# Optimization experiments

Hardware: AMD Instinct MI355X
Metric: run time of the kernel (lower is better)

## Reference

```python
import jax, jax.numpy as jnp
import numpy as np

NV, NF, DIM = 6144, 12288, 256


def _linear(x, W, b):
    # torch nn.Linear: x @ W.T + b, W has shape (out, in)
    return x @ W.T + b


def _agg(X, A, Wf, bf, Wg, bg):
    # AGG: out_fc = Linear(A @ X); out_gagg = Linear(A @ out_fc)  (eval mode: dropout is identity)
    out_fc = _linear(A @ X, Wf, bf)
    out_g = _linear(A @ out_fc, Wg, bg)
    return jax.nn.relu(out_fc + out_g)


def setup_inputs() -> dict:
    key = jax.random.key(0)
    ks = jax.random.split(key, 18)
    primal = jax.random.normal(ks[0], (NV, DIM), jnp.float32)
    # degree-normalized adjacency (docstring): scale uniform entries by 1/N for stable row sums
    A_primal = jax.random.uniform(ks[1], (NV, NV), jnp.float32) * (1.0 / NV)
    A_dual = jax.random.uniform(ks[2], (NF, NF), jnp.float32) * (1.0 / NF)
    A = jax.random.uniform(ks[3], (NV, NF), jnp.float32) * (1.0 / NF)
    faces = jax.random.randint(ks[4], (NF, 3), 0, NV)

    w = lambda k, shp: jax.random.normal(k, shp, jnp.float32) * 0.05
    return {
        "primal": primal, "A_primal": A_primal, "A_dual": A_dual, "A": A, "faces": faces,
        # 3 primal AGG layers (fc + gagg), stacked on leading axis
        "pW": w(ks[5], (3, DIM, DIM)), "pb": w(ks[6], (3, DIM)),
        "pgW": w(ks[7], (3, DIM, DIM)), "pgb": w(ks[8], (3, DIM)),
        # 3 dual AGG layers
        "dW": w(ks[9], (3, DIM, DIM)), "db": w(ks[10], (3, DIM)),
        "dgW": w(ks[11], (3, DIM, DIM)), "dgb": w(ks[12], (3, DIM)),
        # PDF linears: (dim, 2*dim)
        "Wp": w(ks[13], (DIM, 2 * DIM)), "bp": w(ks[14], (DIM,)),
        "Wd": w(ks[15], (DIM, 2 * DIM)), "bd": w(ks[16], (DIM,)),
    }


def reference(primal, A_primal, A_dual, A, faces, pW, pb, pgW, pgb, dW, db, dgW, dgb, Wp, bp, Wd, bd):
    x_p = primal
    x_d = (1.0 / 3.0) * (A.T @ primal)  # primal_dual
    primal_outs, dual_outs = [], []
    for i in range(3):
        primal_outs.append(x_p)
        x_p = _agg(x_p, A_primal, pW[i], pb[i], pgW[i], pgb[i]) + x_p
    for i in range(3):
        dual_outs.append(x_d)
        x_d = _agg(x_d, A_dual, dW[i], db[i], dgW[i], dgb[i]) + x_d
    # PDF: DAP gather-reduce  (N_f, 3, dim) -> (N_f, dim)
    f = jnp.mean(jnp.abs(x_p[faces] - x_d[:, None, :]), axis=1)
    out_dual = jax.nn.relu(_linear(jnp.concatenate([x_d, f], axis=1), Wd, bd))
    mapped = A @ f  # dual_primal
    out_primal = jax.nn.relu(_linear(jnp.concatenate([x_p, mapped], axis=1), Wp, bp))
    return (out_primal + x_p, out_dual + x_d, *primal_outs, *dual_outs)
```

## Files before the change

### kernel.cpp

```cpp
#include <hip/hip_runtime.h>


typedef short short8 __attribute__((ext_vector_type(8)));
typedef float floatx4 __attribute__((ext_vector_type(4)));
typedef unsigned short ushort4v __attribute__((ext_vector_type(4)));
typedef unsigned short u16;

#define DIMN 256
#define GBK 64

static const int kNV = 6144;
static const int kNF = 12288;
static const int SLAB = 768;

#define RW_PW    0
#define RW_PGW   1572864
#define RW_DW    3145728
#define RW_DGW   3932160
#define RW_WCOMB 4718592
#define RW_TOT   5308416

__device__ __forceinline__ float bf2f(u16 u) {
  union { unsigned int i; float f; } x; x.i = ((unsigned int)u) << 16; return x.f;
}
__device__ __forceinline__ u16 f2bf(float f) {
  union { float f; unsigned int i; } x; x.f = f;
  unsigned int r = x.i + 0x7fffu + ((x.i >> 16) & 1u);
  return (u16)(r >> 16);
}
__device__ __forceinline__ void gld_lds16(const void* g, void* l) {
  __builtin_amdgcn_global_load_lds((__attribute__((address_space(1))) void*)(g),
                                   (__attribute__((address_space(3))) void*)(l),
                                   16, 0, 0);
}

__global__ __launch_bounds__(256, 2)
void gemm_bf16_k(const void* __restrict__ A0, int A0is32, size_t aslab0,
                 const void* __restrict__ A1, int A1is32, size_t aslab1, int K1,
                 int lda0, int lda1,
                 const void* __restrict__ Bt, int Btis32, int ldb,
                 void* __restrict__ P, int M, int nx, int kchunk,
                 int fused, const float* __restrict__ bias,
                 const u16* __restrict__ addmat, int do_relu,
                 const float* __restrict__ resid,
                 float* __restrict__ outf, u16* __restrict__ out16)
{
  __shared__ __align__(16) u16 As[2][128 * GBK];
  __shared__ __align__(16) u16 Bs[2][128 * GBK];

  const int nwg = gridDim.x;
  const int d = ((blockIdx.x & 7) * (nwg >> 3)) + (blockIdx.x >> 3);
  const int y = d & 1;
  const int bx = (d >> 1) % nx;
  const int bz = (d >> 1) / nx;
  const int m0 = bx << 7;
  const int n0 = y << 7;
  const int kb = bz * kchunk;
  const int nkt = kchunk / GBK;

  const int tid = threadIdx.x;
  const int wid = tid >> 6;
  const int lane = tid & 63;
  const int wr = wid >> 1, wc = wid & 1;
  const int srow = lane >> 3;
  const int skk = (lane & 7) << 3;

  floatx4 acc[4][4];
  floatx4 zz = {0.f, 0.f, 0.f, 0.f};
#pragma unroll
  for (int i = 0; i < 4; ++i)
#pragma unroll
    for (int j = 0; j < 4; ++j) acc[i][j] = zz;

  auto stage = [&](int buf, int k0) {
    const void* base; int lda, is32, kl; size_t aslab;
    if (k0 < K1) { base = A0; lda = lda0; is32 = A0is32; kl = k0; aslab = aslab0; }
    else { base = A1; lda = lda1; is32 = A1is32; kl = k0 - K1; aslab = aslab1; }
    const size_t koff = aslab ? ((size_t)(kl >> 8) * aslab + (kl & 255)) : (size_t)kl;
    if (is32) {
      const float* F = (const float*)base;
#pragma unroll
      for (int j = 0; j < 4; ++j) {
        int c = (wid << 2) + j;
        const size_t gi = (size_t)(m0 + (c << 3) + srow) * lda + koff + skk;
        floatx4 f0 = *(const floatx4*)(F + gi);
        floatx4 f1 = *(const floatx4*)(F + gi + 4);
        short8 v;
#pragma unroll
        for (int e = 0; e < 4; ++e) { v[e] = (short)f2bf(f0[e]); v[4 + e] = (short)f2bf(f1[e]); }
        *(short8*)&As[buf][(c << 9) + (lane << 3)] = v;
      }
    } else {
      const u16* U = (const u16*)base;
#pragma unroll
      for (int j = 0; j < 4; ++j) {
        int c = (wid << 2) + j;
        gld_lds16(U + (size_t)(m0 + (c << 3) + srow) * lda + koff + skk,
                  (void*)&As[buf][c << 9]);
      }
    }
    if (Btis32) {
      const float* F = (const float*)Bt;
#pragma unroll
      for (int j = 0; j < 4; ++j) {
        int c = (wid << 2) + j;
        const size_t gi = (size_t)(n0 + (c << 3) + srow) * ldb + k0 + skk;
        floatx4 f0 = *(const floatx4*)(F + gi);
        floatx4 f1 = *(const floatx4*)(F + gi + 4);
        short8 v;
#pragma unroll
        for (int e = 0; e < 4; ++e) { v[e] = (short)f2bf(f0[e]); v[4 + e] = (short)f2bf(f1[e]); }
        *(short8*)&Bs[buf][(c << 9) + (lane << 3)] = v;
      }
    } else {
      const u16* U = (const u16*)Bt;
#pragma unroll
      for (int j = 0; j < 4; ++j) {
        int c = (wid << 2) + j;
        gld_lds16(U + (size_t)(n0 + (c << 3) + srow) * ldb + k0 + skk,
                  (void*)&Bs[buf][c << 9]);
      }
    }
  };

  int cur = 0;
  stage(0, kb);
  for (int kt = 0; kt < nkt; ++kt) {
    __syncthreads();
    if (kt + 1 < nkt) stage(cur ^ 1, kb + (kt + 1) * GBK);
#pragma unroll
    for (int ks = 0; ks < 2; ++ks) {
      short8 a[4], b[4];
      const int ko = (ks << 5) + ((lane >> 4) << 3);
#pragma unroll
      for (int mi = 0; mi < 4; ++mi)
        a[mi] = *(const short8*)&As[cur][((wr << 6) + (mi << 4) + (lane & 15)) * GBK + ko];
#pragma unroll
      for (int ni = 0; ni < 4; ++ni)
        b[ni] = *(const short8*)&Bs[cur][((wc << 6) + (ni << 4) + (lane & 15)) * GBK + ko];
#pragma unroll
      for (int mi = 0; mi < 4; ++mi)
#pragma unroll
        for (int ni = 0; ni < 4; ++ni)
          acc[mi][ni] = __builtin_amdgcn_mfma_f32_16x16x32_bf16(a[mi], b[ni], acc[mi][ni], 0, 0, 0);
    }
    cur ^= 1;
  }

  if (fused) {
#pragma unroll
    for (int mi = 0; mi < 4; ++mi) {
#pragma unroll
      for (int ni = 0; ni < 4; ++ni) {
        const int mb = m0 + (wr << 6) + (mi << 4) + ((lane >> 4) << 2);
        const int n = n0 + (wc << 6) + (ni << 4) + (lane & 15);
        const float bv = bias ? bias[n] : 0.f;
#pragma unroll
        for (int r = 0; r < 4; ++r) {
          const size_t idx = (size_t)(mb + r) * DIMN + n;
          float t = acc[mi][ni][r] + bv;
          if (addmat) t += bf2f(addmat[idx]);
          if (do_relu) t = fmaxf(t, 0.f);
          if (resid) t += resid[idx];
          if (outf) outf[idx] = t;
          if (out16) out16[idx] = f2bf(t);
        }
      }
    }
  } else {
    u16* Pz = (u16*)P + (size_t)bz * (size_t)M * DIMN;
#pragma unroll
    for (int mi = 0; mi < 4; ++mi) {
#pragma unroll
      for (int ni = 0; ni < 4; ++ni) {
        const int mb = m0 + (wr << 6) + (mi << 4) + ((lane >> 4) << 2);
        const int n = n0 + (wc << 6) + (ni << 4) + (lane & 15);
#pragma unroll
        for (int r = 0; r < 4; ++r)
          Pz[(size_t)(mb + r) * DIMN + n] = f2bf(acc[mi][ni][r]);
      }
    }
  }
}

__global__ __launch_bounds__(256)
void finalize_k(const u16* __restrict__ P, int S, int Mrows, float scale,
                float* __restrict__ out, u16* __restrict__ out16)
{
  const size_t MN = (size_t)Mrows * DIMN;
  const size_t i4 = (((size_t)blockIdx.x * blockDim.x) + threadIdx.x) * 4;
  if (i4 >= MN) return;
  floatx4 v = {0.f, 0.f, 0.f, 0.f};
  for (int s = 0; s < S; ++s) {
    ushort4v p4 = *(const ushort4v*)(P + (size_t)s * MN + i4);
#pragma unroll
    for (int j = 0; j < 4; ++j) v[j] += bf2f(p4[j]);
  }
  floatx4 o;
#pragma unroll
  for (int j = 0; j < 4; ++j) o[j] = v[j] * scale;
  if (out) *(floatx4*)(out + i4) = o;
  if (out16) {
    unsigned long long q = 0;
#pragma unroll
    for (int j = 0; j < 4; ++j) q |= ((unsigned long long)f2bf(o[j])) << (16 * j);
    *(unsigned long long*)(out16 + i4) = q;
  }
}

__global__ __launch_bounds__(256)
void finalize_tr_k(const u16* __restrict__ P, int S, int Mrows, float scale,
                   float* __restrict__ outf, u16* __restrict__ outT, int ldT)
{
  __shared__ __align__(16) u16 t[64][64];
  const size_t MN = (size_t)Mrows * DIMN;
  const int r0 = blockIdx.x << 6;
  const int c0 = blockIdx.y << 6;
  const int tid = threadIdx.x;
  const int lr = tid >> 3;
  const int lc = (tid & 7) << 3;
#pragma unroll
  for (int h = 0; h < 2; ++h) {
    const int r = lr + (h << 5);
    const size_t gi = (size_t)(r0 + r) * DIMN + (c0 + lc);
    float a[8];
#pragma unroll
    for (int e = 0; e < 8; ++e) a[e] = 0.f;
    for (int s = 0; s < S; ++s) {
      short8 p = *(const short8*)(P + (size_t)s * MN + gi);
#pragma unroll
      for (int e = 0; e < 8; ++e) a[e] += bf2f((u16)p[e]);
    }
    short8 v;
    floatx4 o0, o1;
#pragma unroll
    for (int e = 0; e < 4; ++e) {
      o0[e] = a[e] * scale; o1[e] = a[4 + e] * scale;
      v[e] = (short)f2bf(o0[e]); v[4 + e] = (short)f2bf(o1[e]);
    }
    *(floatx4*)(outf + gi) = o0;
    *(floatx4*)(outf + gi + 4) = o1;
    *(short8*)&t[r][lc ^ ((r >> 3) << 3)] = v;
  }
  __syncthreads();
#pragma unroll
  for (int h = 0; h < 2; ++h) {
    const int oc = lr + (h << 5);
    short8 v;
#pragma unroll
    for (int e = 0; e < 8; ++e)
      v[e] = (short)t[lc + e][oc ^ ((lc >> 3) << 3)];
    *(short8*)&outT[(size_t)(c0 + oc) * ldT + (r0 + lc)] = v;
  }
}

__global__ __launch_bounds__(256)
void transpose_k(const void* __restrict__ in, int is32, int ldin,
                 u16* __restrict__ out, int ldout, u16* __restrict__ copy16)
{
  __shared__ __align__(16) u16 t[64][64];
  const int c0 = blockIdx.x << 6;
  const int r0 = blockIdx.y << 6;
  const int tid = threadIdx.x;
  const int lr = tid >> 3;
  const int lc = (tid & 7) << 3;
#pragma unroll
  for (int h = 0; h < 2; ++h) {
    const int r = lr + (h << 5);
    short8 v;
    if (is32) {
      const float* F = (const float*)in;
      const size_t gi = (size_t)(r0 + r) * ldin + (c0 + lc);
      floatx4 f0 = *(const floatx4*)(F + gi);
      floatx4 f1 = *(const floatx4*)(F + gi + 4);
#pragma unroll
      for (int e = 0; e < 4; ++e) { v[e] = (short)f2bf(f0[e]); v[4 + e] = (short)f2bf(f1[e]); }
      if (copy16) *(short8*)(copy16 + gi) = v;
    } else {
      v = *(const short8*)((const u16*)in + (size_t)(r0 + r) * ldin + (c0 + lc));
    }
    *(short8*)&t[r][lc ^ ((r >> 3) << 3)] = v;
  }
  __syncthreads();
#pragma unroll
  for (int h = 0; h < 2; ++h) {
    const int oc = lr + (h << 5);
    short8 v;
#pragma unroll
    for (int e = 0; e < 8; ++e)
      v[e] = (short)t[lc + e][oc ^ ((lc >> 3) << 3)];
    *(short8*)&out[(size_t)(c0 + oc) * ldout + (r0 + lc)] = v;
  }
}

__global__ __launch_bounds__(256)
void cvt8_k(const float* __restrict__ in, u16* __restrict__ out, size_t n)
{
  const size_t stride = (size_t)gridDim.x * 2048;
  for (size_t i = (((size_t)blockIdx.x << 8) + threadIdx.x) << 3; i < n; i += stride) {
    floatx4 f0 = *(const floatx4*)(in + i);
    floatx4 f1 = *(const floatx4*)(in + i + 4);
    short8 v;
#pragma unroll
    for (int e = 0; e < 4; ++e) { v[e] = (short)f2bf(f0[e]); v[4 + e] = (short)f2bf(f1[e]); }
    *(short8*)(out + i) = v;
  }
}

__global__ __launch_bounds__(256)
void repw_k(const float* __restrict__ pW, const float* __restrict__ pgW,
            const float* __restrict__ dW, const float* __restrict__ dgW,
            const float* __restrict__ Wp, u16* __restrict__ arena)
{
  const size_t o = (((size_t)blockIdx.x << 8) + threadIdx.x) << 3;
  if (o >= RW_TOT) return;
  const float* src;
  size_t so;
  if (o < RW_PGW) {
    size_t r = o - RW_PW; int i = (int)(r >> 19); int rr = (int)(r & 524287);
    so = (size_t)i * 65536 + (rr >> 11) * 256 + (rr & 255); src = pW;
  } else if (o < RW_DW) {
    size_t r = o - RW_PGW; int i = (int)(r >> 19); int rr = (int)(r & 524287);
    so = (size_t)i * 65536 + (rr >> 11) * 256 + (rr & 255); src = pgW;
  } else if (o < RW_DGW) {
    size_t r = o - RW_DW; int i = (int)(r >> 18); int rr = (int)(r & 262143);
    so = (size_t)i * 65536 + (rr >> 10) * 256 + (rr & 255); src = dW;
  } else if (o < RW_WCOMB) {
    size_t r = o - RW_DGW; int i = (int)(r >> 18); int rr = (int)(r & 262143);
    so = (size_t)i * 65536 + (rr >> 10) * 256 + (rr & 255); src = dgW;
  } else {
    size_t r = o - RW_WCOMB; int n = (int)(r / 2304); int k2 = (int)(r % 2304);
    so = (size_t)n * 512 + ((k2 < 256) ? k2 : (256 + ((k2 - 256) & 255))); src = Wp;
  }
  short8 v;
#pragma unroll
  for (int e = 0; e < 8; ++e) v[e] = (short)f2bf(src[so + e]);
  *(short8*)(arena + o) = v;
}

__global__ __launch_bounds__(256)
void face_gather_k(const float* __restrict__ xp, const float* __restrict__ xd,
                   const int* __restrict__ faces, u16* __restrict__ f)
{
  const int fi = blockIdx.x;
  const int j = threadIdx.x;
  const int a = faces[fi * 3 + 0];
  const int b = faces[fi * 3 + 1];
  const int c = faces[fi * 3 + 2];
  const float xv = xd[(size_t)fi * DIMN + j];
  const float s = fabsf(xp[(size_t)a * DIMN + j] - xv)
                + fabsf(xp[(size_t)b * DIMN + j] - xv)
                + fabsf(xp[(size_t)c * DIMN + j] - xv);
  f[(size_t)fi * DIMN + j] = f2bf(s * (1.0f / 3.0f));
}

extern "C" void kernel_launch(void* const* d_in, const int* in_sizes, int n_in,
                              void* d_out, int out_size, void* d_ws, size_t ws_size,
                              hipStream_t stream)
{
  (void)in_sizes; (void)n_in; (void)out_size;
  const float* primal   = (const float*)d_in[0];
  const float* A_primal = (const float*)d_in[1];
  const float* A_dual   = (const float*)d_in[2];
  const float* A        = (const float*)d_in[3];
  const int* faces      = (const int*)d_in[4];
  const float* pW  = (const float*)d_in[5];
  const float* pb  = (const float*)d_in[6];
  const float* pgW = (const float*)d_in[7];
  const float* pgb = (const float*)d_in[8];
  const float* dW  = (const float*)d_in[9];
  const float* db  = (const float*)d_in[10];
  const float* dgW = (const float*)d_in[11];
  const float* dgb = (const float*)d_in[12];
  const float* Wp  = (const float*)d_in[13];
  const float* bp  = (const float*)d_in[14];
  const float* Wd  = (const float*)d_in[15];
  const float* bd  = (const float*)d_in[16];

  char* wsp = (char*)d_ws;
  auto alloc = [&](size_t bytes) -> void* {
    void* p = (void*)wsp;
    wsp += (bytes + 255) & ~(size_t)255;
    return p;
  };
  const size_t NVD = (size_t)kNV * DIMN, NFD = (size_t)kNF * DIMN;
  u16* XT    = (u16*)alloc(NFD * 2);
  u16* TB    = (u16*)alloc((size_t)SLAB * kNV * 2);
  u16* t1    = (u16*)alloc(NFD * 2);
  u16* fc    = (u16*)alloc(NFD * 2);
  u16* P     = (u16*)alloc((size_t)8 * NFD * 2);
  u16* Wrep  = (u16*)alloc((size_t)RW_TOT * 2);
  const size_t bigElems = (size_t)kNF * kNF + 2 * (size_t)kNF * kNV + (size_t)kNV * kNV;
  const size_t need = (size_t)(wsp - (char*)d_ws) + bigElems * 2 + 4096;
  const bool big = ws_size >= need;
  u16 *Ad16 = nullptr, *At16 = nullptr, *A16 = nullptr, *Ap16 = nullptr;
  if (big) {
    Ad16 = (u16*)alloc((size_t)kNF * kNF * 2);
    At16 = (u16*)alloc((size_t)kNF * kNV * 2);
    A16  = (u16*)alloc((size_t)kNV * kNF * 2);
    Ap16 = (u16*)alloc((size_t)kNV * kNV * 2);
  }

  float* out0  = (float*)d_out;
  float* out1  = out0 + NVD;
  float* pouts = out1 + NFD;
  float* douts = pouts + 3 * NVD;

  auto gemmP = [&](const void* A0p, int a0is32, int lda0,
                   const void* Btp, int ldb, int M, int K, int S) {
    const int nx = M / 128;
    gemm_bf16_k<<<dim3(nx * 2 * S), dim3(256), 0, stream>>>(
        A0p, a0is32, 0, nullptr, 0, 0, K, lda0, 0, Btp, 0, ldb,
        P, M, nx, K / S, 0, nullptr, nullptr, 0, nullptr, nullptr, nullptr);
  };
  auto gemmF = [&](const void* A0p, int a0is32, size_t as0, int lda0,
                   const void* A1p, int a1is32, size_t as1, int lda1, int K1,
                   const void* Btp, int btis32, int ldb, int M, int K,
                   const float* bias, const u16* add, int relu,
                   const float* resid, float* outf, u16* out16) {
    const int nx = M / 128;
    gemm_bf16_k<<<dim3(nx * 2), dim3(256), 0, stream>>>(
        A0p, a0is32, as0, A1p, a1is32, as1, K1, lda0, lda1, Btp, btis32, ldb,
        P, M, nx, K, 1, bias, add, relu, resid, outf, out16);
  };
  auto tranp = [&](const void* in, int is32, int ldin, u16* out, int ldout,
                   int R, int C, u16* copy16) {
    transpose_k<<<dim3(C / 64, R / 64), dim3(256), 0, stream>>>(
        in, is32, ldin, out, ldout, copy16);
  };
  auto cvt = [&](const float* in, u16* out, size_t n) {
    cvt8_k<<<dim3(2048), dim3(256), 0, stream>>>(in, out, n);
  };

  repw_k<<<dim3(RW_TOT / 2048), dim3(256), 0, stream>>>(pW, pgW, dW, dgW, Wp, Wrep);
  if (big) {
    cvt(A_dual, Ad16, (size_t)kNF * kNF);
    cvt(A_primal, Ap16, (size_t)kNV * kNV);
    tranp(A, 1, kNF, At16, kNV, kNV, kNF, A16);
  }
  tranp(primal, 1, DIMN, XT, kNV, kNV, DIMN, nullptr);
  hipMemcpyAsync(pouts, primal, NVD * 4, hipMemcpyDeviceToDevice, stream);

  const void* ApP = big ? (const void*)Ap16 : (const void*)A_primal;
  const int apf = big ? 0 : 1;
  const void* AdP = big ? (const void*)Ad16 : (const void*)A_dual;
  const int adf = big ? 0 : 1;

  const float* xpc = primal;
  for (int i = 0; i < 3; ++i) {
    gemmP(ApP, apf, kNV, XT, kNV, kNV, kNV, 8);
    gemmF(P, 0, NVD, 256, nullptr, 0, 0, 0, 2048,
          Wrep + RW_PW + (size_t)i * 524288, 0, 2048, kNV, 2048,
          pb + i * 256, nullptr, 0, nullptr, nullptr, fc);
    tranp(fc, 0, DIMN, TB, kNV, kNV, DIMN, nullptr);
    gemmP(ApP, apf, kNV, TB, kNV, kNV, kNV, 8);
    float* nxt = (i < 2) ? (pouts + (size_t)(i + 1) * NVD) : out0;
    gemmF(P, 0, NVD, 256, nullptr, 0, 0, 0, 2048,
          Wrep + RW_PGW + (size_t)i * 524288, 0, 2048, kNV, 2048,
          pgb + i * 256, fc, 1, xpc, nxt, nullptr);
    xpc = nxt;
    if (i < 2) tranp(xpc, 1, DIMN, XT, kNV, kNV, DIMN, nullptr);
  }

  if (big) {
    tranp(primal, 1, DIMN, XT, kNV, kNV, DIMN, nullptr);
    gemmP(At16, 0, kNV, XT, kNV, kNF, kNV, 4);
    finalize_tr_k<<<dim3(kNF / 64, 4), dim3(256), 0, stream>>>(
        P, 4, kNF, 1.0f / 3.0f, douts, XT, kNF);
  } else {
    tranp(primal, 1, DIMN, XT, kNV, kNV, DIMN, nullptr);
    for (int s = 0; s < kNF / SLAB; ++s) {
      const int m0 = s * SLAB;
      tranp(A + m0, 1, kNF, TB, kNV, kNV, SLAB, nullptr);
      gemmP(TB, 0, kNV, XT, kNV, SLAB, kNV, 16);
      finalize_k<<<dim3((unsigned)((size_t)SLAB * DIMN / 1024)), dim3(256), 0, stream>>>(
          P, 16, SLAB, 1.0f / 3.0f, douts + (size_t)m0 * DIMN, nullptr);
    }
    tranp(douts, 1, DIMN, XT, kNF, kNF, DIMN, nullptr);
  }

  const float* xdc = douts;
  for (int i = 0; i < 3; ++i) {
    gemmP(AdP, adf, kNF, XT, kNF, kNF, kNF, 4);
    gemmF(P, 0, NFD, 256, nullptr, 0, 0, 0, 1024,
          Wrep + RW_DW + (size_t)i * 262144, 0, 1024, kNF, 1024,
          db + i * 256, nullptr, 0, nullptr, nullptr, fc);
    tranp(fc, 0, DIMN, TB, kNF, kNF, DIMN, nullptr);
    gemmP(AdP, adf, kNF, TB, kNF, kNF, kNF, 4);
    float* nxt = (i < 2) ? (douts + (size_t)(i + 1) * NFD) : out1;
    gemmF(P, 0, NFD, 256, nullptr, 0, 0, 0, 1024,
          Wrep + RW_DGW + (size_t)i * 262144, 0, 1024, kNF, 1024,
          dgb + i * 256, fc, 1, xdc, nxt, nullptr);
    xdc = nxt;
    if (i < 2) tranp(xdc, 1, DIMN, XT, kNF, kNF, DIMN, nullptr);
  }

  face_gather_k<<<dim3(kNF), dim3(256), 0, stream>>>(xpc, xdc, faces, t1);
  tranp(t1, 0, DIMN, TB, kNF, kNF, DIMN, nullptr);
  gemmF(xdc, 1, 0, 256, t1, 0, 0, 256, 256, Wd, 1, 512, kNF, 512,
        bd, nullptr, 1, xdc, out1, nullptr);
  if (big) gemmP(A16, 0, kNF, TB, kNF, kNV, kNF, 8);
  else     gemmP(A, 1, kNF, TB, kNF, kNV, kNF, 8);
  gemmF(xpc, 1, 0, 256, P, 0, NVD, 256, 256,
        Wrep + RW_WCOMB, 0, 2304, kNV, 2304,
        bp, nullptr, 1, xpc, out0, nullptr);
}
```

Measured before the change: 2.206 ms.

## Reduce split-K partials in A-load and fuse transposed output into GEMM epilogue

The linear GEMMs no longer fold the split-K reduction into a replicated-weight K dimension (repw_k removed). They now sum the S bf16 partial slabs while staging the A tile, so K shrinks to 256. The epilogue can also write a transposed bf16 copy through LDS, which removes separate transpose launches for fc and the next-layer X^T. Weights are read as fp32 and converted inline. The cost is more redundant partial reads in the A-load path, since each N-tile rereads the partials, and an extra LDS pass with barriers.

```diff
diff --git a/kernel.cpp b/kernel.cpp
--- a/kernel.cpp
+++ b/kernel.cpp
@@ -13,13 +13,6 @@
 static const int kNF = 12288;
 static const int SLAB = 768;
 
-#define RW_PW    0
-#define RW_PGW   1572864
-#define RW_DW    3145728
-#define RW_DGW   3932160
-#define RW_WCOMB 4718592
-#define RW_TOT   5308416
-
 __device__ __forceinline__ float bf2f(u16 u) {
   union { unsigned int i; float f; } x; x.i = ((unsigned int)u) << 16; return x.f;
 }
@@ -35,15 +28,17 @@
 }
 
 __global__ __launch_bounds__(256, 2)
-void gemm_bf16_k(const void* __restrict__ A0, int A0is32, size_t aslab0,
-                 const void* __restrict__ A1, int A1is32, size_t aslab1, int K1,
-                 int lda0, int lda1,
+void gemm_bf16_k(const void* __restrict__ A0, int A0mode, int A0sum, size_t aslab0,
+                 int lda0,
+                 const void* __restrict__ A1, int A1mode, int A1sum, size_t aslab1,
+                 int lda1, int K1,
                  const void* __restrict__ Bt, int Btis32, int ldb,
-                 void* __restrict__ P, int M, int nx, int kchunk,
+                 u16* __restrict__ P, int M, int nx, int kchunk,
                  int fused, const float* __restrict__ bias,
                  const u16* __restrict__ addmat, int do_relu,
                  const float* __restrict__ resid,
-                 float* __restrict__ outf, u16* __restrict__ out16)
+                 float* __restrict__ outf, u16* __restrict__ out16,
+                 u16* __restrict__ outT)
 {
   __shared__ __align__(16) u16 As[2][128 * GBK];
   __shared__ __align__(16) u16 Bs[2][128 * GBK];
@@ -73,16 +68,23 @@
     for (int j = 0; j < 4; ++j) acc[i][j] = zz;
 
   auto stage = [&](int buf, int k0) {
-    const void* base; int lda, is32, kl; size_t aslab;
-    if (k0 < K1) { base = A0; lda = lda0; is32 = A0is32; kl = k0; aslab = aslab0; }
-    else { base = A1; lda = lda1; is32 = A1is32; kl = k0 - K1; aslab = aslab1; }
-    const size_t koff = aslab ? ((size_t)(kl >> 8) * aslab + (kl & 255)) : (size_t)kl;
-    if (is32) {
-      const float* F = (const float*)base;
+    const void* base; int lda, mode, kl, sum; size_t slab;
+    if (k0 < K1) { base = A0; lda = lda0; mode = A0mode; kl = k0; sum = A0sum; slab = aslab0; }
+    else { base = A1; lda = lda1; mode = A1mode; kl = k0 - K1; sum = A1sum; slab = aslab1; }
+    if (mode == 0) {
+      const u16* U = (const u16*)base;
 #pragma unroll
       for (int j = 0; j < 4; ++j) {
         int c = (wid << 2) + j;
-        const size_t gi = (size_t)(m0 + (c << 3) + srow) * lda + koff + skk;
+        gld_lds16(U + (size_t)(m0 + (c << 3) + srow) * lda + kl + skk,
+                  (void*)&As[buf][c << 9]);
+      }
+    } else if (mode == 1) {
+      const float* F = (const float*)base;
+#pragma unroll
+      for (int j = 0; j < 4; ++j) {
+        int c = (wid << 2) + j;
+        const size_t gi = (size_t)(m0 + (c << 3) + srow) * lda + kl + skk;
         floatx4 f0 = *(const floatx4*)(F + gi);
         floatx4 f1 = *(const floatx4*)(F + gi + 4);
         short8 v;
@@ -91,12 +93,23 @@
         *(short8*)&As[buf][(c << 9) + (lane << 3)] = v;
       }
     } else {
-      const u16* U = (const u16*)base;
+      const u16* Pb = (const u16*)base;
 #pragma unroll
       for (int j = 0; j < 4; ++j) {
         int c = (wid << 2) + j;
-        gld_lds16(U + (size_t)(m0 + (c << 3) + srow) * lda + koff + skk,
-                  (void*)&As[buf][c << 9]);
+        const size_t gi = (size_t)(m0 + (c << 3) + srow) * lda + kl + skk;
+        float a[8];
+#pragma unroll
+        for (int e = 0; e < 8; ++e) a[e] = 0.f;
+        for (int s = 0; s < sum; ++s) {
+          short8 p = *(const short8*)(Pb + (size_t)s * slab + gi);
+#pragma unroll
+          for (int e = 0; e < 8; ++e) a[e] += bf2f((u16)p[e]);
+        }
+        short8 v;
+#pragma unroll
+        for (int e = 0; e < 8; ++e) v[e] = (short)f2bf(a[e]);
+        *(short8*)&As[buf][(c << 9) + (lane << 3)] = v;
       }
     }
     if (Btis32) {
@@ -148,27 +161,47 @@
   }
 
   if (fused) {
+    u16* ts = (u16*)&As[0][0];
+    if (outT) __syncthreads();
 #pragma unroll
     for (int mi = 0; mi < 4; ++mi) {
 #pragma unroll
       for (int ni = 0; ni < 4; ++ni) {
-        const int mb = m0 + (wr << 6) + (mi << 4) + ((lane >> 4) << 2);
-        const int n = n0 + (wc << 6) + (ni << 4) + (lane & 15);
+        const int ml0 = (wr << 6) + (mi << 4) + ((lane >> 4) << 2);
+        const int nl = (wc << 6) + (ni << 4) + (lane & 15);
+        const int n = n0 + nl;
         const float bv = bias ? bias[n] : 0.f;
 #pragma unroll
         for (int r = 0; r < 4; ++r) {
-          const size_t idx = (size_t)(mb + r) * DIMN + n;
+          const int ml = ml0 + r;
+          const size_t idx = (size_t)(m0 + ml) * DIMN + n;
           float t = acc[mi][ni][r] + bv;
           if (addmat) t += bf2f(addmat[idx]);
           if (do_relu) t = fmaxf(t, 0.f);
           if (resid) t += resid[idx];
           if (outf) outf[idx] = t;
-          if (out16) out16[idx] = f2bf(t);
+          const u16 q = f2bf(t);
+          if (out16) out16[idx] = q;
+          if (outT) ts[ml * 128 + (nl ^ ((ml & 7) << 3))] = q;
         }
       }
     }
+    if (outT) {
+      __syncthreads();
+      const int nl = tid >> 1;
+      const int mh = (tid & 1) << 6;
+#pragma unroll
+      for (int c8 = 0; c8 < 8; ++c8) {
+        const int mB = mh + (c8 << 3);
+        short8 v;
+#pragma unroll
+        for (int e = 0; e < 8; ++e)
+          v[e] = (short)ts[(mB + e) * 128 + (nl ^ (((mB + e) & 7) << 3))];
+        *(short8*)&outT[(size_t)(n0 + nl) * M + (m0 + mB)] = v;
+      }
+    }
   } else {
-    u16* Pz = (u16*)P + (size_t)bz * (size_t)M * DIMN;
+    u16* Pz = P + (size_t)bz * (size_t)M * DIMN;
 #pragma unroll
     for (int mi = 0; mi < 4; ++mi) {
 #pragma unroll
@@ -305,37 +338,6 @@
     for (int e = 0; e < 4; ++e) { v[e] = (short)f2bf(f0[e]); v[4 + e] = (short)f2bf(f1[e]); }
     *(short8*)(out + i) = v;
   }
-}
-
-__global__ __launch_bounds__(256)
-void repw_k(const float* __restrict__ pW, const float* __restrict__ pgW,
-            const float* __restrict__ dW, const float* __restrict__ dgW,
-            const float* __restrict__ Wp, u16* __restrict__ arena)
-{
-  const size_t o = (((size_t)blockIdx.x << 8) + threadIdx.x) << 3;
-  if (o >= RW_TOT) return;
-  const float* src;
-  size_t so;
-  if (o < RW_PGW) {
-    size_t r = o - RW_PW; int i = (int)(r >> 19); int rr = (int)(r & 524287);
-    so = (size_t)i * 65536 + (rr >> 11) * 256 + (rr & 255); src = pW;
-  } else if (o < RW_DW) {
-    size_t r = o - RW_PGW; int i = (int)(r >> 19); int rr = (int)(r & 524287);
-    so = (size_t)i * 65536 + (rr >> 11) * 256 + (rr & 255); src = pgW;
-  } else if (o < RW_DGW) {
-    size_t r = o - RW_DW; int i = (int)(r >> 18); int rr = (int)(r & 262143);
-    so = (size_t)i * 65536 + (rr >> 10) * 256 + (rr & 255); src = dW;
-  } else if (o < RW_WCOMB) {
-    size_t r = o - RW_DGW; int i = (int)(r >> 18); int rr = (int)(r & 262143);
-    so = (size_t)i * 65536 + (rr >> 10) * 256 + (rr & 255); src = dgW;
-  } else {
-    size_t r = o - RW_WCOMB; int n = (int)(r / 2304); int k2 = (int)(r % 2304);
-    so = (size_t)n * 512 + ((k2 < 256) ? k2 : (256 + ((k2 - 256) & 255))); src = Wp;
-  }
-  short8 v;
-#pragma unroll
-  for (int e = 0; e < 8; ++e) v[e] = (short)f2bf(src[so + e]);
-  *(short8*)(arena + o) = v;
 }
 
 __global__ __launch_bounds__(256)
@@ -384,12 +386,14 @@
     return p;
   };
   const size_t NVD = (size_t)kNV * DIMN, NFD = (size_t)kNF * DIMN;
-  u16* XT    = (u16*)alloc(NFD * 2);
-  u16* TB    = (u16*)alloc((size_t)SLAB * kNV * 2);
+  u16* XTp   = (u16*)alloc(NVD * 2);
+  u16* XTd   = (u16*)alloc(NFD * 2);
+  u16* TB    = (u16*)alloc(NFD * 2);
   u16* t1    = (u16*)alloc(NFD * 2);
   u16* fc    = (u16*)alloc(NFD * 2);
+  float* xp3 = (float*)alloc(NVD * 4);
+  float* xd3 = (float*)alloc(NFD * 4);
   u16* P     = (u16*)alloc((size_t)8 * NFD * 2);
-  u16* Wrep  = (u16*)alloc((size_t)RW_TOT * 2);
   const size_t bigElems = (size_t)kNF * kNF + 2 * (size_t)kNF * kNV + (size_t)kNV * kNV;
   const size_t need = (size_t)(wsp - (char*)d_ws) + bigElems * 2 + 4096;
   const bool big = ws_size >= need;
@@ -406,22 +410,22 @@
   float* pouts = out1 + NFD;
   float* douts = pouts + 3 * NVD;
 
-  auto gemmP = [&](const void* A0p, int a0is32, int lda0,
-                   const void* Btp, int ldb, int M, int K, int S) {
+  auto gemmP = [&](const void* A0p, int a0mode, int lda0,
+                   const u16* Btp, int ldb, int M, int K, int S) {
     const int nx = M / 128;
     gemm_bf16_k<<<dim3(nx * 2 * S), dim3(256), 0, stream>>>(
-        A0p, a0is32, 0, nullptr, 0, 0, K, lda0, 0, Btp, 0, ldb,
-        P, M, nx, K / S, 0, nullptr, nullptr, 0, nullptr, nullptr, nullptr);
+        A0p, a0mode, 0, 0, lda0, nullptr, 0, 0, 0, 0, K, Btp, 0, ldb,
+        P, M, nx, K / S, 0, nullptr, nullptr, 0, nullptr, nullptr, nullptr, nullptr);
   };
-  auto gemmF = [&](const void* A0p, int a0is32, size_t as0, int lda0,
-                   const void* A1p, int a1is32, size_t as1, int lda1, int K1,
-                   const void* Btp, int btis32, int ldb, int M, int K,
+  auto gemmF = [&](const void* A0p, int a0mode, int a0sum, size_t as0, int lda0,
+                   const void* A1p, int a1mode, int a1sum, size_t as1, int lda1,
+                   int K1, const void* Btp, int btis32, int ldb, int M, int K,
                    const float* bias, const u16* add, int relu,
-                   const float* resid, float* outf, u16* out16) {
+                   const float* resid, float* outf, u16* out16, u16* outT) {
     const int nx = M / 128;
     gemm_bf16_k<<<dim3(nx * 2), dim3(256), 0, stream>>>(
-        A0p, a0is32, as0, A1p, a1is32, as1, K1, lda0, lda1, Btp, btis32, ldb,
-        P, M, nx, K, 1, bias, add, relu, resid, outf, out16);
+        A0p, a0mode, a0sum, as0, lda0, A1p, a1mode, a1sum, as1, lda1, K1,
+        Btp, btis32, ldb, P, M, nx, K, 1, bias, add, relu, resid, outf, out16, outT);
   };
   auto tranp = [&](const void* in, int is32, int ldin, u16* out, int ldout,
                    int R, int C, u16* copy16) {
@@ -432,76 +436,70 @@
     cvt8_k<<<dim3(2048), dim3(256), 0, stream>>>(in, out, n);
   };
 
-  repw_k<<<dim3(RW_TOT / 2048), dim3(256), 0, stream>>>(pW, pgW, dW, dgW, Wp, Wrep);
   if (big) {
     cvt(A_dual, Ad16, (size_t)kNF * kNF);
     cvt(A_primal, Ap16, (size_t)kNV * kNV);
     tranp(A, 1, kNF, At16, kNV, kNV, kNF, A16);
   }
-  tranp(primal, 1, DIMN, XT, kNV, kNV, DIMN, nullptr);
+  tranp(primal, 1, DIMN, XTp, kNV, kNV, DIMN, nullptr);
   hipMemcpyAsync(pouts, primal, NVD * 4, hipMemcpyDeviceToDevice, stream);
 
-  const void* ApP = big ? (const void*)Ap16 : (const void*)A_primal;
-  const int apf = big ? 0 : 1;
-  const void* AdP = big ? (const void*)Ad16 : (const void*)A_dual;
-  const int adf = big ? 0 : 1;
-
-  const float* xpc = primal;
-  for (int i = 0; i < 3; ++i) {
-    gemmP(ApP, apf, kNV, XT, kNV, kNV, kNV, 8);
-    gemmF(P, 0, NVD, 256, nullptr, 0, 0, 0, 2048,
-          Wrep + RW_PW + (size_t)i * 524288, 0, 2048, kNV, 2048,
-          pb + i * 256, nullptr, 0, nullptr, nullptr, fc);
-    tranp(fc, 0, DIMN, TB, kNV, kNV, DIMN, nullptr);
-    gemmP(ApP, apf, kNV, TB, kNV, kNV, kNV, 8);
-    float* nxt = (i < 2) ? (pouts + (size_t)(i + 1) * NVD) : out0;
-    gemmF(P, 0, NVD, 256, nullptr, 0, 0, 0, 2048,
-          Wrep + RW_PGW + (size_t)i * 524288, 0, 2048, kNV, 2048,
-          pgb + i * 256, fc, 1, xpc, nxt, nullptr);
-    xpc = nxt;
-    if (i < 2) tranp(xpc, 1, DIMN, XT, kNV, kNV, DIMN, nullptr);
-  }
-
   if (big) {
-    tranp(primal, 1, DIMN, XT, kNV, kNV, DIMN, nullptr);
-    gemmP(At16, 0, kNV, XT, kNV, kNF, kNV, 4);
+    gemmP(At16, 0, kNV, XTp, kNV, kNF, kNV, 4);
     finalize_tr_k<<<dim3(kNF / 64, 4), dim3(256), 0, stream>>>(
-        P, 4, kNF, 1.0f / 3.0f, douts, XT, kNF);
+        P, 4, kNF, 1.0f / 3.0f, douts, XTd, kNF);
   } else {
-    tranp(primal, 1, DIMN, XT, kNV, kNV, DIMN, nullptr);
     for (int s = 0; s < kNF / SLAB; ++s) {
       const int m0 = s * SLAB;
       tranp(A + m0, 1, kNF, TB, kNV, kNV, SLAB, nullptr);
-      gemmP(TB, 0, kNV, XT, kNV, SLAB, kNV, 16);
+      gemmP(TB, 0, kNV, XTp, kNV, SLAB, kNV, 16);
       finalize_k<<<dim3((unsigned)((size_t)SLAB * DIMN / 1024)), dim3(256), 0, stream>>>(
           P, 16, SLAB, 1.0f / 3.0f, douts + (size_t)m0 * DIMN, nullptr);
     }
-    tranp(douts, 1, DIMN, XT, kNF, kNF, DIMN, nullptr);
+    tranp(douts, 1, DIMN, XTd, kNF, kNF, DIMN, nullptr);
+  }
+
+  const void* ApP = big ? (const void*)Ap16 : (const void*)A_primal;
+  const int apm = big ? 0 : 1;
+  const void* AdP = big ? (const void*)Ad16 : (const void*)A_dual;
+  const int adm = big ? 0 : 1;
+
+  const float* xpc = primal;
+  for (int i = 0; i < 3; ++i) {
+    gemmP(ApP, apm, kNV, XTp, kNV, kNV, kNV, 8);
+    gemmF(P, 2, 8, NVD, 256, nullptr, 0, 0, 0, 0, 256,
+          pW + (size_t)i * 65536, 1, 256, kNV, 256,
+          pb + i * 256, nullptr, 0, nullptr, nullptr, fc, TB);
+    gemmP(ApP, apm, kNV, TB, kNV, kNV, kNV, 8);
+    float* nxt = (i < 2) ? (pouts + (size_t)(i + 1) * NVD) : xp3;
+    u16* xtT = (i < 2) ? XTp : nullptr;
+    gemmF(P, 2, 8, NVD, 256, nullptr, 0, 0, 0, 0, 256,
+          pgW + (size_t)i * 65536, 1, 256, kNV, 256,
+          pgb + i * 256, fc, 1, xpc, nxt, nullptr, xtT);
+    xpc = nxt;
   }
 
   const float* xdc = douts;
   for (int i = 0; i < 3; ++i) {
-    gemmP(AdP, adf, kNF, XT, kNF, kNF, kNF, 4);
-    gemmF(P, 0, NFD, 256, nullptr, 0, 0, 0, 1024,
-          Wrep + RW_DW + (size_t)i * 262144, 0, 1024, kNF, 1024,
-          db + i * 256, nullptr, 0, nullptr, nullptr, fc);
-    tranp(fc, 0, DIMN, TB, kNF, kNF, DIMN, nullptr);
-    gemmP(AdP, adf, kNF, TB, kNF, kNF, kNF, 4);
-    float* nxt = (i < 2) ? (douts + (size_t)(i + 1) * NFD) : out1;
-    gemmF(P, 0, NFD, 256, nullptr, 0, 0, 0, 1024,
-          Wrep + RW_DGW + (size_t)i * 262144, 0, 1024, kNF, 1024,
-          dgb + i * 256, fc, 1, xdc, nxt, nullptr);
+    gemmP(AdP, adm, kNF, XTd, kNF, kNF, kNF, 4);
+    gemmF(P, 2, 4, NFD, 256, nullptr, 0, 0, 0, 0, 256,
+          dW + (size_t)i * 65536, 1, 256, kNF, 256,
+          db + i * 256, nullptr, 0, nullptr, nullptr, fc, TB);
+    gemmP(AdP, adm, kNF, TB, kNF, kNF, kNF, 4);
+    float* nxt = (i < 2) ? (douts + (size_t)(i + 1) * NFD) : xd3;
+    u16* xtT = (i < 2) ? XTd : nullptr;
+    gemmF(P, 2, 4, NFD, 256, nullptr, 0, 0, 0, 0, 256,
+          dgW + (size_t)i * 65536, 1, 256, kNF, 256,
+          dgb + i * 256, fc, 1, xdc, nxt, nullptr, xtT);
     xdc = nxt;
-    if (i < 2) tranp(xdc, 1, DIMN, XT, kNF, kNF, DIMN, nullptr);
-  }
-
-  face_gather_k<<<dim3(kNF), dim3(256), 0, stream>>>(xpc, xdc, faces, t1);
+  }
+
+  face_gather_k<<<dim3(kNF), dim3(256), 0, stream>>>(xp3, xd3, faces, t1);
   tranp(t1, 0, DIMN, TB, kNF, kNF, DIMN, nullptr);
-  gemmF(xdc, 1, 0, 256, t1, 0, 0, 256, 256, Wd, 1, 512, kNF, 512,
-        bd, nullptr, 1, xdc, out1, nullptr);
+  gemmF(xd3, 1, 0, 0, 256, t1, 0, 0, 0, 256, 256, Wd, 1, 512, kNF, 512,
+        bd, nullptr, 1, xd3, out1, nullptr, nullptr);
   if (big) gemmP(A16, 0, kNF, TB, kNF, kNV, kNF, 8);
   else     gemmP(A, 1, kNF, TB, kNF, kNV, kNF, 8);
-  gemmF(xpc, 1, 0, 256, P, 0, NVD, 256, 256,
-        Wrep + RW_WCOMB, 0, 2304, kNV, 2304,
-        bp, nullptr, 1, xpc, out0, nullptr);
-}
+  gemmF(xp3, 1, 0, 0, 256, P, 2, 8, NVD, 256, 256, Wp, 1, 512, kNV, 512,
+        bp, nullptr, 1, xp3, out0, nullptr, nullptr);
+}
```

Result: slower. 2.324 ms (+5.3%).
